# Optimization experiments

Hardware: AMD Instinct MI355X
Metric: run time of the kernel (lower is better)

The kernel has to match this reference:

```python
import jax, jax.numpy as jnp
import numpy as np

B, N, C, H = 2, 1024, 1024, 16
HD = C // H
SCALE = HD ** -0.5
TEMPERATURE = 0.8
TOP_K = 64
TOP_P = 0.9
NKAT_STRENGTH = 0.5
NKAT_DECAY = 0.95
LAYER_IDX = 2
NEG = jnp.float32(-1e9)  # stand-in for -inf; exp underflows to 0 after max-subtract


def setup_inputs() -> dict:
    key = jax.random.key(0)
    k0, k1, k2, k3 = jax.random.split(key, 4)
    x = jax.random.normal(k0, (B, N, C), dtype=jnp.float32)
    w_qkv = jax.random.normal(k1, (C, 3 * C), dtype=jnp.float32) * 0.02
    w_out = jax.random.normal(k2, (C, C), dtype=jnp.float32) * 0.02
    b_out = jnp.zeros((C,), dtype=jnp.float32)
    nkat_alpha = jnp.float32(0.1)
    nkat_beta = jnp.float32(0.05)
    return {"x": x, "w_qkv": w_qkv, "w_out": w_out, "b_out": b_out,
            "nkat_alpha": nkat_alpha, "nkat_beta": nkat_beta}


def _nkat_attention(x, w_qkv, w_out, b_out, nkat_alpha, nkat_beta):
    # qkv projection and head split
    qkv = (x @ w_qkv).reshape(B, N, 3, H, HD)
    q = jnp.transpose(qkv[:, :, 0], (0, 2, 1, 3))  # (B,H,N,HD)
    k = jnp.transpose(qkv[:, :, 1], (0, 2, 1, 3))
    v = jnp.transpose(qkv[:, :, 2], (0, 2, 1, 3))

    # scores + (zero) pos_bias + temperature scaling
    scores = jnp.einsum('bhqd,bhkd->bhqk', q, k) * SCALE
    scores = scores / max(TEMPERATURE, 1e-8)

    # top-k filtering: keep only the TOP_K largest scores per query
    kth = jax.lax.top_k(scores, TOP_K)[0][..., -1:]  # (B,H,N,1)
    scores = jnp.where(scores >= kth, scores, NEG)

    # nucleus (top-p) filtering: keep minimal prefix of sorted probs with
    # exclusive cumulative mass <= TOP_P (first element always kept)
    sorted_desc = -jnp.sort(-scores, axis=-1)
    probs = jax.nn.softmax(sorted_desc, axis=-1)
    cum = jnp.cumsum(probs, axis=-1)
    keep = (cum - probs) <= TOP_P  # exclusive cumsum <= p
    thr = jnp.min(jnp.where(keep, sorted_desc, jnp.inf), axis=-1, keepdims=True)
    scores = jnp.where(scores >= thr, scores, NEG)

    attn = jax.nn.softmax(scores, axis=-1)  # dropout p=0 -> identity (eval)

    # NKAT enhancement: per-token semantic modulation from x statistics
    layer_coeff = NKAT_STRENGTH * NKAT_DECAY ** LAYER_IDX
    token_mean = jnp.mean(x, axis=-1, keepdims=True)              # (B,N,1)
    token_var = jnp.mean((x - token_mean) ** 2, axis=-1, keepdims=True)
    theta = nkat_alpha * jnp.tanh(token_mean) + nkat_beta * jax.nn.sigmoid(token_var)
    attn = attn * (1.0 + layer_coeff * theta[:, None])            # (B,1,N,1) broadcast

    out = jnp.einsum('bhqk,bhkd->bhqd', attn, v)  # (B,H,N,HD)
    out = jnp.transpose(out, (0, 2, 1, 3)).reshape(B, N, C)
    return out @ w_out + b_out


def reference(x, w_qkv, w_out, b_out, nkat_alpha, nkat_beta):
    return _nkat_attention(x, w_qkv, w_out, b_out, nkat_alpha, nkat_beta)
```

## Files before the change

### kernel.cpp

```cpp
#include <hip/hip_runtime.h>

#define B_ 2
#define N_ 1024
#define C_ 1024
#define H_ 16
#define HD_ 64
#define KPAD 36
#define KPADL 40

typedef short short8 __attribute__((ext_vector_type(8)));
typedef float f32x4 __attribute__((ext_vector_type(4)));

union U16 {
  uint4 q;
  unsigned u[4];
  short8 s;
};

__device__ __forceinline__ float wsumf(float x) {
#pragma unroll
  for (int off = 32; off; off >>= 1) x += __shfl_xor(x, off, 64);
  return x;
}
__device__ __forceinline__ unsigned orderu(float f) {
  unsigned b = __float_as_uint(f);
  return (b & 0x80000000u) ? ~b : (b | 0x80000000u);
}
__device__ __forceinline__ float iorderu(unsigned x) {
  unsigned b = (x & 0x80000000u) ? (x & 0x7FFFFFFFu) : ~x;
  return __uint_as_float(b);
}

__device__ __forceinline__ unsigned splitf2(float f) {
  unsigned u = __float_as_uint(f);
  unsigned t = (u + 0x7fffu + ((u >> 16) & 1u)) & 0xffff0000u;
  float r = f - __uint_as_float(t);
  unsigned v = __float_as_uint(r);
  unsigned tv = v + 0x7fffu + ((v >> 16) & 1u);
  return (t >> 16) | (tv & 0xffff0000u);
}
__device__ __forceinline__ void splitf3(float f, unsigned& hm,
                                        unsigned short& lo) {
  unsigned u = __float_as_uint(f);
  unsigned t = (u + 0x7fffu + ((u >> 16) & 1u)) & 0xffff0000u;
  float r1 = f - __uint_as_float(t);
  unsigned v = __float_as_uint(r1);
  unsigned tv = (v + 0x7fffu + ((v >> 16) & 1u)) & 0xffff0000u;
  float r2 = r1 - __uint_as_float(tv);
  unsigned w = __float_as_uint(r2);
  unsigned tw = w + 0x7fffu + ((w >> 16) & 1u);
  hm = (t >> 16) | tv;
  lo = (unsigned short)(tw >> 16);
}

__device__ __forceinline__ void unpack_hm(const unsigned* p, short8& h,
                                          short8& l) {
  const uint4 X = *(const uint4*)p;
  const uint4 Y = *(const uint4*)(p + 4);
  U16 Hh, Ll;
  Hh.u[0] = (X.x & 0xffffu) | (X.y << 16);
  Hh.u[1] = (X.z & 0xffffu) | (X.w << 16);
  Hh.u[2] = (Y.x & 0xffffu) | (Y.y << 16);
  Hh.u[3] = (Y.z & 0xffffu) | (Y.w << 16);
  Ll.u[0] = (X.x >> 16) | (X.y & 0xffff0000u);
  Ll.u[1] = (X.z >> 16) | (X.w & 0xffff0000u);
  Ll.u[2] = (Y.x >> 16) | (Y.y & 0xffff0000u);
  Ll.u[3] = (Y.z >> 16) | (Y.w & 0xffff0000u);
  h = Hh.s;
  l = Ll.s;
}

__global__ __launch_bounds__(64) void factor_kernel(
    const float* __restrict__ x, const float* __restrict__ alpha_p,
    const float* __restrict__ beta_p, float* __restrict__ fac) {
  const int row = blockIdx.x;
  const int lane = threadIdx.x;
  const float4* xr = (const float4*)(x + (size_t)row * C_);
  float s = 0.f, ss = 0.f;
#pragma unroll
  for (int j = 0; j < 4; ++j) {
    float4 v = xr[lane + 64 * j];
    s += v.x + v.y + v.z + v.w;
    ss += v.x * v.x + v.y * v.y + v.z * v.z + v.w * v.w;
  }
  s = wsumf(s);
  ss = wsumf(ss);
  const float mean = s * (1.f / 1024.f);
  const float var = ss * (1.f / 1024.f) - mean * mean;
  const float theta =
      alpha_p[0] * tanhf(mean) + beta_p[0] * (1.f / (1.f + __expf(-var)));
  if (lane == 0) fac[row] = 1.f + 0.45125f * theta;
}

__device__ __forceinline__ void mfma_core6(
    const float* __restrict__ A, const float* __restrict__ Bm, int lda,
    int ldb, int m0, int n0, unsigned* a_hm, unsigned* b_hm,
    unsigned short* a_lo, unsigned short* b_lo, f32x4 acc[4][4]) {
  const int tid = threadIdx.x;
  const int lane = tid & 63;
  const int wm = ((tid >> 7) & 1) * 64;
  const int wn = ((tid >> 6) & 1) * 64;
  const int a_k4 = (tid & 7) * 4, a_m = tid >> 3;
  const int b_n4 = (tid & 31) * 4, b_k = (tid >> 5) * 4;
  const int fr = lane & 15, fk = (lane >> 4) * 8;

  float4 aR[4], bR[4];
#pragma unroll
  for (int j = 0; j < 4; ++j)
    aR[j] = *(const float4*)(A + (size_t)(m0 + a_m + 32 * j) * lda + a_k4);
#pragma unroll
  for (int i = 0; i < 4; ++i)
    bR[i] = *(const float4*)(Bm + (size_t)(b_k + i) * ldb + n0 + b_n4);

  for (int kt = 0; kt < 32; ++kt) {
    __syncthreads();
#pragma unroll
    for (int j = 0; j < 4; ++j) {
      uint4 w;
      ushort4 l;
      splitf3(aR[j].x, w.x, l.x);
      splitf3(aR[j].y, w.y, l.y);
      splitf3(aR[j].z, w.z, l.z);
      splitf3(aR[j].w, w.w, l.w);
      *(uint4*)(a_hm + (a_m + 32 * j) * KPAD + a_k4) = w;
      *(ushort4*)(a_lo + (a_m + 32 * j) * KPADL + a_k4) = l;
    }
#pragma unroll
    for (int i = 0; i < 4; ++i) {
      unsigned hm;
      unsigned short lo;
      splitf3(bR[i].x, hm, lo);
      b_hm[(b_n4 + 0) * KPAD + b_k + i] = hm;
      b_lo[(b_n4 + 0) * KPADL + b_k + i] = lo;
      splitf3(bR[i].y, hm, lo);
      b_hm[(b_n4 + 1) * KPAD + b_k + i] = hm;
      b_lo[(b_n4 + 1) * KPADL + b_k + i] = lo;
      splitf3(bR[i].z, hm, lo);
      b_hm[(b_n4 + 2) * KPAD + b_k + i] = hm;
      b_lo[(b_n4 + 2) * KPADL + b_k + i] = lo;
      splitf3(bR[i].w, hm, lo);
      b_hm[(b_n4 + 3) * KPAD + b_k + i] = hm;
      b_lo[(b_n4 + 3) * KPADL + b_k + i] = lo;
    }
    __syncthreads();
    if (kt + 1 < 32) {
      const int kb = (kt + 1) * 32;
#pragma unroll
      for (int j = 0; j < 4; ++j)
        aR[j] =
            *(const float4*)(A + (size_t)(m0 + a_m + 32 * j) * lda + kb + a_k4);
#pragma unroll
      for (int i = 0; i < 4; ++i)
        bR[i] = *(const float4*)(Bm + (size_t)(kb + b_k + i) * ldb + n0 + b_n4);
    }
    short8 ah[4], am[4], al[4];
#pragma unroll
    for (int rt = 0; rt < 4; ++rt) {
      const int row = wm + rt * 16 + fr;
      unpack_hm(a_hm + row * KPAD + fk, ah[rt], am[rt]);
      U16 L;
      L.q = *(const uint4*)(a_lo + row * KPADL + fk);
      al[rt] = L.s;
    }
#pragma unroll
    for (int ct = 0; ct < 4; ++ct) {
      const int row = wn + ct * 16 + fr;
      short8 bh, bm, bl;
      unpack_hm(b_hm + row * KPAD + fk, bh, bm);
      U16 L;
      L.q = *(const uint4*)(b_lo + row * KPADL + fk);
      bl = L.s;
#pragma unroll
      for (int rt = 0; rt < 4; ++rt) {
        f32x4 c = acc[rt][ct];
        c = __builtin_amdgcn_mfma_f32_16x16x32_bf16(ah[rt], bl, c, 0, 0, 0);
        c = __builtin_amdgcn_mfma_f32_16x16x32_bf16(al[rt], bh, c, 0, 0, 0);
        c = __builtin_amdgcn_mfma_f32_16x16x32_bf16(am[rt], bm, c, 0, 0, 0);
        c = __builtin_amdgcn_mfma_f32_16x16x32_bf16(ah[rt], bm, c, 0, 0, 0);
        c = __builtin_amdgcn_mfma_f32_16x16x32_bf16(am[rt], bh, c, 0, 0, 0);
        c = __builtin_amdgcn_mfma_f32_16x16x32_bf16(ah[rt], bh, c, 0, 0, 0);
        acc[rt][ct] = c;
      }
    }
  }
}

__device__ __forceinline__ void mfma_core3(const float* __restrict__ A,
                                           const float* __restrict__ Bm,
                                           int lda, int ldb, int m0, int n0,
                                           unsigned* a_hm, unsigned* b_hm,
                                           f32x4 acc[4][4]) {
  const int tid = threadIdx.x;
  const int lane = tid & 63;
  const int wm = ((tid >> 7) & 1) * 64;
  const int wn = ((tid >> 6) & 1) * 64;
  const int a_k4 = (tid & 7) * 4, a_m = tid >> 3;
  const int b_n4 = (tid & 31) * 4, b_k = (tid >> 5) * 4;
  const int fr = lane & 15, fk = (lane >> 4) * 8;

  float4 aR[4], bR[4];
#pragma unroll
  for (int j = 0; j < 4; ++j)
    aR[j] = *(const float4*)(A + (size_t)(m0 + a_m + 32 * j) * lda + a_k4);
#pragma unroll
  for (int i = 0; i < 4; ++i)
    bR[i] = *(const float4*)(Bm + (size_t)(b_k + i) * ldb + n0 + b_n4);

  for (int kt = 0; kt < 32; ++kt) {
    __syncthreads();
#pragma unroll
    for (int j = 0; j < 4; ++j) {
      uint4 w;
      w.x = splitf2(aR[j].x);
      w.y = splitf2(aR[j].y);
      w.z = splitf2(aR[j].z);
      w.w = splitf2(aR[j].w);
      *(uint4*)(a_hm + (a_m + 32 * j) * KPAD + a_k4) = w;
    }
#pragma unroll
    for (int i = 0; i < 4; ++i) {
      unsigned* bp = b_hm + b_k + i;
      bp[(b_n4 + 0) * KPAD] = splitf2(bR[i].x);
      bp[(b_n4 + 1) * KPAD] = splitf2(bR[i].y);
      bp[(b_n4 + 2) * KPAD] = splitf2(bR[i].z);
      bp[(b_n4 + 3) * KPAD] = splitf2(bR[i].w);
    }
    __syncthreads();
    if (kt + 1 < 32) {
      const int kb = (kt + 1) * 32;
#pragma unroll
      for (int j = 0; j < 4; ++j)
        aR[j] =
            *(const float4*)(A + (size_t)(m0 + a_m + 32 * j) * lda + kb + a_k4);
#pragma unroll
      for (int i = 0; i < 4; ++i)
        bR[i] = *(const float4*)(Bm + (size_t)(kb + b_k + i) * ldb + n0 + b_n4);
    }
    short8 ah[4], al[4];
#pragma unroll
    for (int rt = 0; rt < 4; ++rt)
      unpack_hm(a_hm + (wm + rt * 16 + fr) * KPAD + fk, ah[rt], al[rt]);
#pragma unroll
    for (int ct = 0; ct < 4; ++ct) {
      short8 bh, bl;
      unpack_hm(b_hm + (wn + ct * 16 + fr) * KPAD + fk, bh, bl);
#pragma unroll
      for (int rt = 0; rt < 4; ++rt) {
        f32x4 c = acc[rt][ct];
        c = __builtin_amdgcn_mfma_f32_16x16x32_bf16(ah[rt], bl, c, 0, 0, 0);
        c = __builtin_amdgcn_mfma_f32_16x16x32_bf16(al[rt], bh, c, 0, 0, 0);
        c = __builtin_amdgcn_mfma_f32_16x16x32_bf16(ah[rt], bh, c, 0, 0, 0);
        acc[rt][ct] = c;
      }
    }
  }
}

__global__ __launch_bounds__(256) void gemm_qk_kernel(
    const float* __restrict__ x, const float* __restrict__ w,
    float* __restrict__ q, float* __restrict__ ktb) {
  __shared__ unsigned a_hm[128 * KPAD];
  __shared__ unsigned b_hm[128 * KPAD];
  __shared__ unsigned short a_lo[128 * KPADL];
  __shared__ unsigned short b_lo[128 * KPADL];
  f32x4 acc[4][4];
#pragma unroll
  for (int i = 0; i < 4; ++i)
#pragma unroll
    for (int j = 0; j < 4; ++j) acc[i][j] = (f32x4){0.f, 0.f, 0.f, 0.f};
  const int m0 = blockIdx.y * 128, n0 = blockIdx.x * 128;
  mfma_core6(x, w, C_, 3 * C_, m0, n0, a_hm, b_hm, a_lo, b_lo, acc);

  const int lane = threadIdx.x & 63;
  const int wm = ((threadIdx.x >> 7) & 1) * 64;
  const int wn = ((threadIdx.x >> 6) & 1) * 64;
  const int rbase = (lane >> 4) * 4, cc = lane & 15;
#pragma unroll
  for (int rt = 0; rt < 4; ++rt) {
    const int m = m0 + wm + rt * 16 + rbase;
    const int bb = m >> 10, nn = m & 1023;
#pragma unroll
    for (int ct = 0; ct < 4; ++ct) {
      const int j = n0 + wn + ct * 16 + cc;
      const int sel = j >> 10, hh = (j >> 6) & 15, d0 = j & 63;
      const f32x4 c = acc[rt][ct];
      if (sel == 1) {
        *(float4*)(ktb + (((size_t)(bb * 16 + hh) * HD_ + d0) << 10) + nn) =
            make_float4(c[0], c[1], c[2], c[3]);
      } else {
        float* dst = q + (((size_t)(bb * 16 + hh) << 10) + nn) * HD_ + d0;
        dst[0] = c[0];
        dst[HD_] = c[1];
        dst[2 * HD_] = c[2];
        dst[3 * HD_] = c[3];
      }
    }
  }
}

__global__ __launch_bounds__(256) void gemm_v_kernel(
    const float* __restrict__ x, const float* __restrict__ w,
    float* __restrict__ v) {
  __shared__ unsigned a_hm[128 * KPAD];
  __shared__ unsigned b_hm[128 * KPAD];
  f32x4 acc[4][4];
#pragma unroll
  for (int i = 0; i < 4; ++i)
#pragma unroll
    for (int j = 0; j < 4; ++j) acc[i][j] = (f32x4){0.f, 0.f, 0.f, 0.f};
  const int m0 = blockIdx.y * 128, n0 = 2048 + blockIdx.x * 128;
  mfma_core3(x, w, C_, 3 * C_, m0, n0, a_hm, b_hm, acc);

  const int lane = threadIdx.x & 63;
  const int wm = ((threadIdx.x >> 7) & 1) * 64;
  const int wn = ((threadIdx.x >> 6) & 1) * 64;
  const int rbase = (lane >> 4) * 4, cc = lane & 15;
#pragma unroll
  for (int rt = 0; rt < 4; ++rt) {
    const int m = m0 + wm + rt * 16 + rbase;
    const int bb = m >> 10, nn = m & 1023;
#pragma unroll
    for (int ct = 0; ct < 4; ++ct) {
      const int jv = (n0 - 2048) + wn + ct * 16 + cc;
      const int hh = (jv >> 6) & 15, d0 = jv & 63;
      const f32x4 c = acc[rt][ct];
      float* dst = v + (((size_t)(bb * 16 + hh) << 10) + nn) * HD_ + d0;
      dst[0] = c[0];
      dst[HD_] = c[1];
      dst[2 * HD_] = c[2];
      dst[3 * HD_] = c[3];
    }
  }
}

__global__ __launch_bounds__(256) void gemm_out_kernel(
    const float* __restrict__ a, const float* __restrict__ w,
    const float* __restrict__ bias, float* __restrict__ out) {
  __shared__ unsigned a_hm[128 * KPAD];
  __shared__ unsigned b_hm[128 * KPAD];
  f32x4 acc[4][4];
#pragma unroll
  for (int i = 0; i < 4; ++i)
#pragma unroll
    for (int j = 0; j < 4; ++j) acc[i][j] = (f32x4){0.f, 0.f, 0.f, 0.f};
  const int m0 = blockIdx.y * 128, n0 = blockIdx.x * 128;
  mfma_core3(a, w, C_, C_, m0, n0, a_hm, b_hm, acc);

  const int lane = threadIdx.x & 63;
  const int wm = ((threadIdx.x >> 7) & 1) * 64;
  const int wn = ((threadIdx.x >> 6) & 1) * 64;
  const int rbase = (lane >> 4) * 4, cc = lane & 15;
#pragma unroll
  for (int rt = 0; rt < 4; ++rt) {
    const int m = m0 + wm + rt * 16 + rbase;
#pragma unroll
    for (int ct = 0; ct < 4; ++ct) {
      const int j = n0 + wn + ct * 16 + cc;
      const float bj = bias[j];
      const f32x4 c = acc[rt][ct];
      float* dst = out + (size_t)m * C_ + j;
      dst[0] = c[0] + bj;
      dst[C_] = c[1] + bj;
      dst[2 * C_] = c[2] + bj;
      dst[3 * C_] = c[3] + bj;
    }
  }
}

__global__ __launch_bounds__(256) void attn_kernel(
    const float* __restrict__ qw, const float* __restrict__ kt,
    const float* __restrict__ vw, const float* __restrict__ fac,
    float* __restrict__ ao) {
  const int lane = threadIdx.x & 63;
  const int wid = threadIdx.x >> 6;
  const int qblk = blockIdx.x * 16;
  const int bh = qblk >> 10;
  const int b = bh >> 4, h = bh & 15;
  const int q0 = (qblk & (N_ - 1)) + wid * 4;

  __shared__ __align__(16) float q_ldsT[4][HD_][4];
  __shared__ unsigned su[4][64];
  __shared__ float sv[4][64];
  __shared__ int ck[4][64];
  __shared__ float cv[4][64];

  {
    const int qq = lane >> 4, dp = (lane & 15) << 2;
    const float4 v =
        *(const float4*)(qw + ((size_t)bh * N_ + q0 + qq) * HD_ + dp);
    q_ldsT[wid][dp + 0][qq] = v.x;
    q_ldsT[wid][dp + 1][qq] = v.y;
    q_ldsT[wid][dp + 2][qq] = v.z;
    q_ldsT[wid][dp + 3][qq] = v.w;
  }

  const float* ktb = kt + ((size_t)bh * HD_ * N_);
  const unsigned long long ltmask = (1ull << lane) - 1ull;
  unsigned u[4][16];

  for (int pass = 0; pass < 4; ++pass) {
    float acc[4][4];
#pragma unroll
    for (int a = 0; a < 4; ++a)
#pragma unroll
      for (int c = 0; c < 4; ++c) acc[a][c] = 0.f;
    const float* kp = ktb + (pass << 8) + (lane << 2);
#pragma unroll 4
    for (int d = 0; d < HD_; ++d) {
      const float4 kv = *(const float4*)(kp + (size_t)d * N_);
      const float4 qv = *(const float4*)(&q_ldsT[wid][d][0]);
      acc[0][0] = fmaf(kv.x, qv.x, acc[0][0]);
      acc[0][1] = fmaf(kv.x, qv.y, acc[0][1]);
      acc[0][2] = fmaf(kv.x, qv.z, acc[0][2]);
      acc[0][3] = fmaf(kv.x, qv.w, acc[0][3]);
      acc[1][0] = fmaf(kv.y, qv.x, acc[1][0]);
      acc[1][1] = fmaf(kv.y, qv.y, acc[1][1]);
      acc[1][2] = fmaf(kv.y, qv.z, acc[1][2]);
      acc[1][3] = fmaf(kv.y, qv.w, acc[1][3]);
      acc[2][0] = fmaf(kv.z, qv.x, acc[2][0]);
      acc[2][1] = fmaf(kv.z, qv.y, acc[2][1]);
      acc[2][2] = fmaf(kv.z, qv.z, acc[2][2]);
      acc[2][3] = fmaf(kv.z, qv.w, acc[2][3]);
      acc[3][0] = fmaf(kv.w, qv.x, acc[3][0]);
      acc[3][1] = fmaf(kv.w, qv.y, acc[3][1]);
      acc[3][2] = fmaf(kv.w, qv.z, acc[3][2]);
      acc[3][3] = fmaf(kv.w, qv.w, acc[3][3]);
    }
#pragma unroll
    for (int jl = 0; jl < 4; ++jl)
#pragma unroll
      for (int q = 0; q < 4; ++q)
        u[q][(pass << 2) + jl] = orderu((acc[jl][q] * 0.125f) / 0.8f);
  }

  unsigned mu[4], l0[4];
#pragma unroll
  for (int q = 0; q < 4; ++q) {
    unsigned mq = u[q][0];
#pragma unroll
    for (int j = 1; j < 16; ++j) mq = max(mq, u[q][j]);
    mu[q] = mq;
    l0[q] = mq;
  }
#pragma unroll
  for (int off = 32; off; off >>= 1) {
#pragma unroll
    for (int q = 0; q < 4; ++q) {
      mu[q] = max(mu[q], (unsigned)__shfl_xor((int)mu[q], off, 64));
      l0[q] = min(l0[q], (unsigned)__shfl_xor((int)l0[q], off, 64));
    }
  }

  unsigned lo[4], hi[4];
#pragma unroll
  for (int q = 0; q < 4; ++q) {
    lo[q] = l0[q];
    hi[q] = mu[q];
  }
  while ((lo[0] < hi[0]) | (lo[1] < hi[1]) | (lo[2] < hi[2]) |
         (lo[3] < hi[3])) {
#pragma unroll
    for (int q = 0; q < 4; ++q) {
      if (lo[q] < hi[q]) {
        const unsigned mid = lo[q] + ((hi[q] - lo[q]) >> 1) + 1u;
        int c = 0;
#pragma unroll
        for (int j = 0; j < 16; ++j)
          c += (int)__popcll(__ballot(u[q][j] >= mid));
        if (c >= 64) lo[q] = mid;
        else hi[q] = mid - 1u;
      }
    }
  }

  const float* vb = vw + ((size_t)bh << 16);
#pragma unroll
  for (int qq = 0; qq < 4; ++qq) {
    const unsigned kthu = lo[qq];
    const float m = iorderu(mu[qq]);

    float e[16];
    float zl = 0.f;
#pragma unroll
    for (int j = 0; j < 16; ++j) {
      const float ej = (u[qq][j] >= kthu) ? __expf(iorderu(u[qq][j]) - m) : 0.f;
      e[j] = ej;
      zl += ej;
    }
    const float Z = wsumf(zl);
    const float limit = 0.9f * Z;

    int base = 0;
#pragma unroll
    for (int j = 0; j < 16; ++j) {
      const bool f = (u[qq][j] >= kthu);
      const unsigned long long mb = __ballot(f);
      if (f) {
        const int pos = base + (int)__popcll(mb & ltmask);
        if (pos < 64) {
          su[wid][pos] = u[qq][j];
          sv[wid][pos] = e[j];
        }
      }
      base += (int)__popcll(mb);
    }

    unsigned sk = ~su[wid][lane];
    float se = sv[wid][lane];
#pragma unroll
    for (int k = 2; k <= 64; k <<= 1) {
#pragma unroll
      for (int j = k >> 1; j; j >>= 1) {
        const unsigned pk = (unsigned)__shfl_xor((int)sk, j, 64);
        const float pe = __shfl_xor(se, j, 64);
        const bool takeMin = (((lane & j) == 0) == ((lane & k) == 0));
        const bool sw = takeMin ? (pk < sk) : (pk > sk);
        if (sw) {
          sk = pk;
          se = pe;
        }
      }
    }

    float pre = se;
#pragma unroll
    for (int off = 1; off <= 32; off <<= 1) {
      const float t = __shfl_up(pre, off, 64);
      if (lane >= off) pre += t;
    }
    const float excl = pre - se;
    const bool keep = (excl <= limit);
    const unsigned long long km = __ballot(keep);
    const int L = 63 - __builtin_clzll(km);
    const unsigned thr = ~(unsigned)__shfl((int)sk, L, 64);

    float z2l = 0.f;
#pragma unroll
    for (int j = 0; j < 16; ++j) z2l += (u[qq][j] >= thr) ? e[j] : 0.f;
    const float Z2 = wsumf(z2l);
    const float wsc = fac[(b << 10) + q0 + qq] / Z2;

    int M = 0;
#pragma unroll
    for (int j = 0; j < 16; ++j) {
      const bool f = (u[qq][j] >= thr);
      const unsigned long long mb = __ballot(f);
      if (f) {
        const int pos = M + (int)__popcll(mb & ltmask);
        if (pos < 64) {
          ck[wid][pos] = ((j >> 2) << 8) + (lane << 2) + (j & 3);
          cv[wid][pos] = e[j] * wsc;
        }
      }
      M += (int)__popcll(mb);
    }
    if (M > 64) M = 64;

    float a0 = 0.f, a1 = 0.f, a2 = 0.f, a3 = 0.f;
    int i = 0;
    for (; i + 4 <= M; i += 4) {
      const int k0 = ck[wid][i], k1 = ck[wid][i + 1];
      const int k2 = ck[wid][i + 2], k3 = ck[wid][i + 3];
      const float c0 = cv[wid][i], c1 = cv[wid][i + 1];
      const float c2 = cv[wid][i + 2], c3 = cv[wid][i + 3];
      a0 = fmaf(c0, vb[((size_t)k0 << 6) + lane], a0);
      a1 = fmaf(c1, vb[((size_t)k1 << 6) + lane], a1);
      a2 = fmaf(c2, vb[((size_t)k2 << 6) + lane], a2);
      a3 = fmaf(c3, vb[((size_t)k3 << 6) + lane], a3);
    }
    for (; i < M; ++i)
      a0 = fmaf(cv[wid][i], vb[((size_t)ck[wid][i] << 6) + lane], a0);
    const float o = (a0 + a1) + (a2 + a3);

    ao[(((size_t)b << 10) + q0 + qq) * C_ + (h << 6) + lane] = o;
  }
}

extern "C" void kernel_launch(void* const* d_in, const int* in_sizes, int n_in,
                              void* d_out, int out_size, void* d_ws,
                              size_t ws_size, hipStream_t stream) {
  const float* x = (const float*)d_in[0];
  const float* wqkv = (const float*)d_in[1];
  const float* wout = (const float*)d_in[2];
  const float* bout = (const float*)d_in[3];
  const float* alpha = (const float*)d_in[4];
  const float* beta = (const float*)d_in[5];
  float* out = (float*)d_out;

  float* ws = (float*)d_ws;
  const size_t SZ = (size_t)B_ * H_ * N_ * HD_;
  float* qw = ws;
  float* kt = ws + SZ;
  float* vw = ws + 2 * SZ;
  float* ao = ws + 3 * SZ;
  float* fc = ws + 4 * SZ;

  factor_kernel<<<B_ * N_, 64, 0, stream>>>(x, alpha, beta, fc);
  gemm_qk_kernel<<<dim3(16, 16), 256, 0, stream>>>(x, wqkv, qw, kt);
  gemm_v_kernel<<<dim3(8, 16), 256, 0, stream>>>(x, wqkv, vw);
  attn_kernel<<<(B_ * H_ * N_) / 16, 256, 0, stream>>>(qw, kt, vw, fc, ao);
  gemm_out_kernel<<<dim3(8, 16), 256, 0, stream>>>(ao, wout, bout, out);
}
```

Baseline: 447.3 us.

## Pre-split fp32 operands into bf16 planes before the GEMMs

Adds separate kernels that split x and the transposed weights into high/mid/low bf16 planes once, so the GEMM main loops only copy ready-made bf16 tiles into shared memory instead of splitting and scattering fp32 values per tile. The attention kernel now writes its output directly as two bf16 planes for the output projection. This removes repeated split arithmetic and the strided shared-memory transpose stores from the GEMM inner loops. The cost is extra kernel launches and extra global traffic to write and reread the split planes, plus a larger workspace layout with buffers reused through aliasing.

```diff
diff --git a/kernel.cpp b/kernel.cpp
--- a/kernel.cpp
+++ b/kernel.cpp
@@ -5,17 +5,11 @@
 #define C_ 1024
 #define H_ 16
 #define HD_ 64
-#define KPAD 36
-#define KPADL 40
+#define PK 40
 
 typedef short short8 __attribute__((ext_vector_type(8)));
 typedef float f32x4 __attribute__((ext_vector_type(4)));
-
-union U16 {
-  uint4 q;
-  unsigned u[4];
-  short8 s;
-};
+typedef unsigned short ushort_t;
 
 __device__ __forceinline__ float wsumf(float x) {
 #pragma unroll
@@ -39,8 +33,7 @@
   unsigned tv = v + 0x7fffu + ((v >> 16) & 1u);
   return (t >> 16) | (tv & 0xffff0000u);
 }
-__device__ __forceinline__ void splitf3(float f, unsigned& hm,
-                                        unsigned short& lo) {
+__device__ __forceinline__ void splitf3(float f, unsigned& hm, ushort_t& lo) {
   unsigned u = __float_as_uint(f);
   unsigned t = (u + 0x7fffu + ((u >> 16) & 1u)) & 0xffff0000u;
   float r1 = f - __uint_as_float(t);
@@ -50,24 +43,7 @@
   unsigned w = __float_as_uint(r2);
   unsigned tw = w + 0x7fffu + ((w >> 16) & 1u);
   hm = (t >> 16) | tv;
-  lo = (unsigned short)(tw >> 16);
-}
-
-__device__ __forceinline__ void unpack_hm(const unsigned* p, short8& h,
-                                          short8& l) {
-  const uint4 X = *(const uint4*)p;
-  const uint4 Y = *(const uint4*)(p + 4);
-  U16 Hh, Ll;
-  Hh.u[0] = (X.x & 0xffffu) | (X.y << 16);
-  Hh.u[1] = (X.z & 0xffffu) | (X.w << 16);
-  Hh.u[2] = (Y.x & 0xffffu) | (Y.y << 16);
-  Hh.u[3] = (Y.z & 0xffffu) | (Y.w << 16);
-  Ll.u[0] = (X.x >> 16) | (X.y & 0xffff0000u);
-  Ll.u[1] = (X.z >> 16) | (X.w & 0xffff0000u);
-  Ll.u[2] = (Y.x >> 16) | (Y.y & 0xffff0000u);
-  Ll.u[3] = (Y.z >> 16) | (Y.w & 0xffff0000u);
-  h = Hh.s;
-  l = Ll.s;
+  lo = (ushort_t)(tw >> 16);
 }
 
 __global__ __launch_bounds__(64) void factor_kernel(
@@ -92,203 +68,173 @@
   if (lane == 0) fac[row] = 1.f + 0.45125f * theta;
 }
 
-__device__ __forceinline__ void mfma_core6(
-    const float* __restrict__ A, const float* __restrict__ Bm, int lda,
-    int ldb, int m0, int n0, unsigned* a_hm, unsigned* b_hm,
-    unsigned short* a_lo, unsigned short* b_lo, f32x4 acc[4][4]) {
+__global__ __launch_bounds__(256) void split_x_kernel(
+    const float* __restrict__ x, ushort_t* __restrict__ xh,
+    ushort_t* __restrict__ xm, ushort_t* __restrict__ xl) {
+  const int i = (blockIdx.x * 256 + threadIdx.x) * 4;
+  const float4 v = *(const float4*)(x + i);
+  unsigned hm0, hm1, hm2, hm3;
+  ushort_t l0, l1, l2, l3;
+  splitf3(v.x, hm0, l0);
+  splitf3(v.y, hm1, l1);
+  splitf3(v.z, hm2, l2);
+  splitf3(v.w, hm3, l3);
+  *(ushort4*)(xh + i) =
+      make_ushort4(hm0 & 0xffffu, hm1 & 0xffffu, hm2 & 0xffffu, hm3 & 0xffffu);
+  *(ushort4*)(xm + i) =
+      make_ushort4(hm0 >> 16, hm1 >> 16, hm2 >> 16, hm3 >> 16);
+  *(ushort4*)(xl + i) = make_ushort4(l0, l1, l2, l3);
+}
+
+__global__ __launch_bounds__(256) void split_wT_kernel(
+    const float* __restrict__ src, int ldsrc, ushort_t* __restrict__ th,
+    ushort_t* __restrict__ tm, ushort_t* __restrict__ tl) {
+  __shared__ float tile[64][65];
+  const int t = threadIdx.x;
+  const int k0 = blockIdx.y * 64, j0 = blockIdx.x * 64;
+  const int rr = t >> 4, cc4 = (t & 15) * 4;
+#pragma unroll
+  for (int p = 0; p < 4; ++p) {
+    const float4 v =
+        *(const float4*)(src + (size_t)(k0 + rr + 16 * p) * ldsrc + j0 + cc4);
+    tile[rr + 16 * p][cc4 + 0] = v.x;
+    tile[rr + 16 * p][cc4 + 1] = v.y;
+    tile[rr + 16 * p][cc4 + 2] = v.z;
+    tile[rr + 16 * p][cc4 + 3] = v.w;
+  }
+  __syncthreads();
+  const int j = t >> 2, kc = (t & 3) * 16;
+#pragma unroll
+  for (int half = 0; half < 2; ++half) {
+    unsigned hw[4], mw[4], lw[4];
+#pragma unroll
+    for (int e = 0; e < 4; ++e) {
+      unsigned hmA, hmB;
+      ushort_t loA, loB;
+      splitf3(tile[kc + half * 8 + 2 * e][j], hmA, loA);
+      splitf3(tile[kc + half * 8 + 2 * e + 1][j], hmB, loB);
+      hw[e] = (hmA & 0xffffu) | ((hmB & 0xffffu) << 16);
+      mw[e] = (hmA >> 16) | (hmB & 0xffff0000u);
+      lw[e] = (unsigned)loA | ((unsigned)loB << 16);
+    }
+    const size_t o = (size_t)(j0 + j) * 1024 + k0 + kc + half * 8;
+    *(uint4*)(th + o) = make_uint4(hw[0], hw[1], hw[2], hw[3]);
+    *(uint4*)(tm + o) = make_uint4(mw[0], mw[1], mw[2], mw[3]);
+    *(uint4*)(tl + o) = make_uint4(lw[0], lw[1], lw[2], lw[3]);
+  }
+}
+
+__global__ __launch_bounds__(256) void gemm_qk_kernel(
+    const ushort_t* __restrict__ xh, const ushort_t* __restrict__ xm,
+    const ushort_t* __restrict__ xl, const ushort_t* __restrict__ wh,
+    const ushort_t* __restrict__ wm, const ushort_t* __restrict__ wl,
+    float* __restrict__ q, float* __restrict__ ktb) {
+  __shared__ ushort_t Ah[128 * PK], Am[128 * PK], Al[128 * PK];
+  __shared__ ushort_t Bh[128 * PK], Bm2[128 * PK], Bl[128 * PK];
+  f32x4 acc[4][4];
+#pragma unroll
+  for (int i = 0; i < 4; ++i)
+#pragma unroll
+    for (int j = 0; j < 4; ++j) acc[i][j] = (f32x4){0.f, 0.f, 0.f, 0.f};
   const int tid = threadIdx.x;
   const int lane = tid & 63;
-  const int wm = ((tid >> 7) & 1) * 64;
-  const int wn = ((tid >> 6) & 1) * 64;
-  const int a_k4 = (tid & 7) * 4, a_m = tid >> 3;
-  const int b_n4 = (tid & 31) * 4, b_k = (tid >> 5) * 4;
+  const int m0 = blockIdx.y * 128, n0 = blockIdx.x * 128;
+  const int wro = ((tid >> 7) & 1) * 64;
+  const int wco = ((tid >> 6) & 1) * 64;
+  const int srow = tid >> 1, soff = (tid & 1) * 16;
   const int fr = lane & 15, fk = (lane >> 4) * 8;
-
-  float4 aR[4], bR[4];
-#pragma unroll
-  for (int j = 0; j < 4; ++j)
-    aR[j] = *(const float4*)(A + (size_t)(m0 + a_m + 32 * j) * lda + a_k4);
-#pragma unroll
-  for (int i = 0; i < 4; ++i)
-    bR[i] = *(const float4*)(Bm + (size_t)(b_k + i) * ldb + n0 + b_n4);
-
+  const size_t ga = (size_t)(m0 + srow) * 1024 + soff;
+  const size_t gb = (size_t)(n0 + srow) * 1024 + soff;
+
+  uint4 aR[3][2], bR[3][2];
+  aR[0][0] = *(const uint4*)(xh + ga);
+  aR[0][1] = *(const uint4*)(xh + ga + 8);
+  aR[1][0] = *(const uint4*)(xm + ga);
+  aR[1][1] = *(const uint4*)(xm + ga + 8);
+  aR[2][0] = *(const uint4*)(xl + ga);
+  aR[2][1] = *(const uint4*)(xl + ga + 8);
+  bR[0][0] = *(const uint4*)(wh + gb);
+  bR[0][1] = *(const uint4*)(wh + gb + 8);
+  bR[1][0] = *(const uint4*)(wm + gb);
+  bR[1][1] = *(const uint4*)(wm + gb + 8);
+  bR[2][0] = *(const uint4*)(wl + gb);
+  bR[2][1] = *(const uint4*)(wl + gb + 8);
+
+  const int lbase = srow * PK + soff;
   for (int kt = 0; kt < 32; ++kt) {
     __syncthreads();
-#pragma unroll
-    for (int j = 0; j < 4; ++j) {
-      uint4 w;
-      ushort4 l;
-      splitf3(aR[j].x, w.x, l.x);
-      splitf3(aR[j].y, w.y, l.y);
-      splitf3(aR[j].z, w.z, l.z);
-      splitf3(aR[j].w, w.w, l.w);
-      *(uint4*)(a_hm + (a_m + 32 * j) * KPAD + a_k4) = w;
-      *(ushort4*)(a_lo + (a_m + 32 * j) * KPADL + a_k4) = l;
-    }
-#pragma unroll
-    for (int i = 0; i < 4; ++i) {
-      unsigned hm;
-      unsigned short lo;
-      splitf3(bR[i].x, hm, lo);
-      b_hm[(b_n4 + 0) * KPAD + b_k + i] = hm;
-      b_lo[(b_n4 + 0) * KPADL + b_k + i] = lo;
-      splitf3(bR[i].y, hm, lo);
-      b_hm[(b_n4 + 1) * KPAD + b_k + i] = hm;
-      b_lo[(b_n4 + 1) * KPADL + b_k + i] = lo;
-      splitf3(bR[i].z, hm, lo);
-      b_hm[(b_n4 + 2) * KPAD + b_k + i] = hm;
-      b_lo[(b_n4 + 2) * KPADL + b_k + i] = lo;
-      splitf3(bR[i].w, hm, lo);
-      b_hm[(b_n4 + 3) * KPAD + b_k + i] = hm;
-      b_lo[(b_n4 + 3) * KPADL + b_k + i] = lo;
-    }
+    *(uint4*)&Ah[lbase] = aR[0][0];
+    *(uint4*)&Ah[lbase + 8] = aR[0][1];
+    *(uint4*)&Am[lbase] = aR[1][0];
+    *(uint4*)&Am[lbase + 8] = aR[1][1];
+    *(uint4*)&Al[lbase] = aR[2][0];
+    *(uint4*)&Al[lbase + 8] = aR[2][1];
+    *(uint4*)&Bh[lbase] = bR[0][0];
+    *(uint4*)&Bh[lbase + 8] = bR[0][1];
+    *(uint4*)&Bm2[lbase] = bR[1][0];
+    *(uint4*)&Bm2[lbase + 8] = bR[1][1];
+    *(uint4*)&Bl[lbase] = bR[2][0];
+    *(uint4*)&Bl[lbase + 8] = bR[2][1];
     __syncthreads();
     if (kt + 1 < 32) {
-      const int kb = (kt + 1) * 32;
-#pragma unroll
-      for (int j = 0; j < 4; ++j)
-        aR[j] =
-            *(const float4*)(A + (size_t)(m0 + a_m + 32 * j) * lda + kb + a_k4);
-#pragma unroll
-      for (int i = 0; i < 4; ++i)
-        bR[i] = *(const float4*)(Bm + (size_t)(kb + b_k + i) * ldb + n0 + b_n4);
-    }
-    short8 ah[4], am[4], al[4];
+      const size_t oa = ga + (size_t)(kt + 1) * 32;
+      const size_t ob = gb + (size_t)(kt + 1) * 32;
+      aR[0][0] = *(const uint4*)(xh + oa);
+      aR[0][1] = *(const uint4*)(xh + oa + 8);
+      aR[1][0] = *(const uint4*)(xm + oa);
+      aR[1][1] = *(const uint4*)(xm + oa + 8);
+      aR[2][0] = *(const uint4*)(xl + oa);
+      aR[2][1] = *(const uint4*)(xl + oa + 8);
+      bR[0][0] = *(const uint4*)(wh + ob);
+      bR[0][1] = *(const uint4*)(wh + ob + 8);
+      bR[1][0] = *(const uint4*)(wm + ob);
+      bR[1][1] = *(const uint4*)(wm + ob + 8);
+      bR[2][0] = *(const uint4*)(wl + ob);
+      bR[2][1] = *(const uint4*)(wl + ob + 8);
+    }
+    short8 fah[4], fam[4], fal[4];
 #pragma unroll
     for (int rt = 0; rt < 4; ++rt) {
-      const int row = wm + rt * 16 + fr;
-      unpack_hm(a_hm + row * KPAD + fk, ah[rt], am[rt]);
-      U16 L;
-      L.q = *(const uint4*)(a_lo + row * KPADL + fk);
-      al[rt] = L.s;
+      const int ba = (wro + rt * 16 + fr) * PK + fk;
+      fah[rt] = *(const short8*)&Ah[ba];
+      fam[rt] = *(const short8*)&Am[ba];
+      fal[rt] = *(const short8*)&Al[ba];
     }
 #pragma unroll
     for (int ct = 0; ct < 4; ++ct) {
-      const int row = wn + ct * 16 + fr;
-      short8 bh, bm, bl;
-      unpack_hm(b_hm + row * KPAD + fk, bh, bm);
-      U16 L;
-      L.q = *(const uint4*)(b_lo + row * KPADL + fk);
-      bl = L.s;
+      const int bb = (wco + ct * 16 + fr) * PK + fk;
+      const short8 fbh = *(const short8*)&Bh[bb];
+      const short8 fbm = *(const short8*)&Bm2[bb];
+      const short8 fbl = *(const short8*)&Bl[bb];
 #pragma unroll
       for (int rt = 0; rt < 4; ++rt) {
         f32x4 c = acc[rt][ct];
-        c = __builtin_amdgcn_mfma_f32_16x16x32_bf16(ah[rt], bl, c, 0, 0, 0);
-        c = __builtin_amdgcn_mfma_f32_16x16x32_bf16(al[rt], bh, c, 0, 0, 0);
-        c = __builtin_amdgcn_mfma_f32_16x16x32_bf16(am[rt], bm, c, 0, 0, 0);
-        c = __builtin_amdgcn_mfma_f32_16x16x32_bf16(ah[rt], bm, c, 0, 0, 0);
-        c = __builtin_amdgcn_mfma_f32_16x16x32_bf16(am[rt], bh, c, 0, 0, 0);
-        c = __builtin_amdgcn_mfma_f32_16x16x32_bf16(ah[rt], bh, c, 0, 0, 0);
+        c = __builtin_amdgcn_mfma_f32_16x16x32_bf16(fah[rt], fbl, c, 0, 0, 0);
+        c = __builtin_amdgcn_mfma_f32_16x16x32_bf16(fal[rt], fbh, c, 0, 0, 0);
+        c = __builtin_amdgcn_mfma_f32_16x16x32_bf16(fam[rt], fbm, c, 0, 0, 0);
+        c = __builtin_amdgcn_mfma_f32_16x16x32_bf16(fah[rt], fbm, c, 0, 0, 0);
+        c = __builtin_amdgcn_mfma_f32_16x16x32_bf16(fam[rt], fbh, c, 0, 0, 0);
+        c = __builtin_amdgcn_mfma_f32_16x16x32_bf16(fah[rt], fbh, c, 0, 0, 0);
         acc[rt][ct] = c;
       }
     }
   }
-}
-
-__device__ __forceinline__ void mfma_core3(const float* __restrict__ A,
-                                           const float* __restrict__ Bm,
-                                           int lda, int ldb, int m0, int n0,
-                                           unsigned* a_hm, unsigned* b_hm,
-                                           f32x4 acc[4][4]) {
-  const int tid = threadIdx.x;
-  const int lane = tid & 63;
-  const int wm = ((tid >> 7) & 1) * 64;
-  const int wn = ((tid >> 6) & 1) * 64;
-  const int a_k4 = (tid & 7) * 4, a_m = tid >> 3;
-  const int b_n4 = (tid & 31) * 4, b_k = (tid >> 5) * 4;
-  const int fr = lane & 15, fk = (lane >> 4) * 8;
-
-  float4 aR[4], bR[4];
-#pragma unroll
-  for (int j = 0; j < 4; ++j)
-    aR[j] = *(const float4*)(A + (size_t)(m0 + a_m + 32 * j) * lda + a_k4);
-#pragma unroll
-  for (int i = 0; i < 4; ++i)
-    bR[i] = *(const float4*)(Bm + (size_t)(b_k + i) * ldb + n0 + b_n4);
-
-  for (int kt = 0; kt < 32; ++kt) {
-    __syncthreads();
-#pragma unroll
-    for (int j = 0; j < 4; ++j) {
-      uint4 w;
-      w.x = splitf2(aR[j].x);
-      w.y = splitf2(aR[j].y);
-      w.z = splitf2(aR[j].z);
-      w.w = splitf2(aR[j].w);
-      *(uint4*)(a_hm + (a_m + 32 * j) * KPAD + a_k4) = w;
-    }
-#pragma unroll
-    for (int i = 0; i < 4; ++i) {
-      unsigned* bp = b_hm + b_k + i;
-      bp[(b_n4 + 0) * KPAD] = splitf2(bR[i].x);
-      bp[(b_n4 + 1) * KPAD] = splitf2(bR[i].y);
-      bp[(b_n4 + 2) * KPAD] = splitf2(bR[i].z);
-      bp[(b_n4 + 3) * KPAD] = splitf2(bR[i].w);
-    }
-    __syncthreads();
-    if (kt + 1 < 32) {
-      const int kb = (kt + 1) * 32;
-#pragma unroll
-      for (int j = 0; j < 4; ++j)
-        aR[j] =
-            *(const float4*)(A + (size_t)(m0 + a_m + 32 * j) * lda + kb + a_k4);
-#pragma unroll
-      for (int i = 0; i < 4; ++i)
-        bR[i] = *(const float4*)(Bm + (size_t)(kb + b_k + i) * ldb + n0 + b_n4);
-    }
-    short8 ah[4], al[4];
-#pragma unroll
-    for (int rt = 0; rt < 4; ++rt)
-      unpack_hm(a_hm + (wm + rt * 16 + fr) * KPAD + fk, ah[rt], al[rt]);
+
+  const int rbase = (lane >> 4) * 4, cc = lane & 15;
+#pragma unroll
+  for (int rt = 0; rt < 4; ++rt) {
+    const int m = m0 + wro + rt * 16 + rbase;
+    const int bb2 = m >> 10, nn = m & 1023;
 #pragma unroll
     for (int ct = 0; ct < 4; ++ct) {
-      short8 bh, bl;
-      unpack_hm(b_hm + (wn + ct * 16 + fr) * KPAD + fk, bh, bl);
-#pragma unroll
-      for (int rt = 0; rt < 4; ++rt) {
-        f32x4 c = acc[rt][ct];
-        c = __builtin_amdgcn_mfma_f32_16x16x32_bf16(ah[rt], bl, c, 0, 0, 0);
-        c = __builtin_amdgcn_mfma_f32_16x16x32_bf16(al[rt], bh, c, 0, 0, 0);
-        c = __builtin_amdgcn_mfma_f32_16x16x32_bf16(ah[rt], bh, c, 0, 0, 0);
-        acc[rt][ct] = c;
-      }
-    }
-  }
-}
-
-__global__ __launch_bounds__(256) void gemm_qk_kernel(
-    const float* __restrict__ x, const float* __restrict__ w,
-    float* __restrict__ q, float* __restrict__ ktb) {
-  __shared__ unsigned a_hm[128 * KPAD];
-  __shared__ unsigned b_hm[128 * KPAD];
-  __shared__ unsigned short a_lo[128 * KPADL];
-  __shared__ unsigned short b_lo[128 * KPADL];
-  f32x4 acc[4][4];
-#pragma unroll
-  for (int i = 0; i < 4; ++i)
-#pragma unroll
-    for (int j = 0; j < 4; ++j) acc[i][j] = (f32x4){0.f, 0.f, 0.f, 0.f};
-  const int m0 = blockIdx.y * 128, n0 = blockIdx.x * 128;
-  mfma_core6(x, w, C_, 3 * C_, m0, n0, a_hm, b_hm, a_lo, b_lo, acc);
-
-  const int lane = threadIdx.x & 63;
-  const int wm = ((threadIdx.x >> 7) & 1) * 64;
-  const int wn = ((threadIdx.x >> 6) & 1) * 64;
-  const int rbase = (lane >> 4) * 4, cc = lane & 15;
-#pragma unroll
-  for (int rt = 0; rt < 4; ++rt) {
-    const int m = m0 + wm + rt * 16 + rbase;
-    const int bb = m >> 10, nn = m & 1023;
-#pragma unroll
-    for (int ct = 0; ct < 4; ++ct) {
-      const int j = n0 + wn + ct * 16 + cc;
+      const int j = n0 + wco + ct * 16 + cc;
       const int sel = j >> 10, hh = (j >> 6) & 15, d0 = j & 63;
       const f32x4 c = acc[rt][ct];
       if (sel == 1) {
-        *(float4*)(ktb + (((size_t)(bb * 16 + hh) * HD_ + d0) << 10) + nn) =
+        *(float4*)(ktb + (((size_t)(bb2 * 16 + hh) * HD_ + d0) << 10) + nn) =
             make_float4(c[0], c[1], c[2], c[3]);
       } else {
-        float* dst = q + (((size_t)(bb * 16 + hh) << 10) + nn) * HD_ + d0;
+        float* dst = q + (((size_t)(bb2 * 16 + hh) << 10) + nn) * HD_ + d0;
         dst[0] = c[0];
         dst[HD_] = c[1];
         dst[2 * HD_] = c[2];
@@ -298,30 +244,103 @@
   }
 }
 
+__device__ __forceinline__ void mfma_core3p(
+    const ushort_t* __restrict__ Ahp, const ushort_t* __restrict__ Amp,
+    const ushort_t* __restrict__ Bhp, const ushort_t* __restrict__ Bmp,
+    int m0, int n0, ushort_t* Ah, ushort_t* Am, ushort_t* Bh, ushort_t* Bm2,
+    f32x4 acc[4][4]) {
+  const int tid = threadIdx.x;
+  const int lane = tid & 63;
+  const int wro = ((tid >> 7) & 1) * 64;
+  const int wco = ((tid >> 6) & 1) * 64;
+  const int srow = tid >> 1, soff = (tid & 1) * 16;
+  const int fr = lane & 15, fk = (lane >> 4) * 8;
+  const size_t ga = (size_t)(m0 + srow) * 1024 + soff;
+  const size_t gb = (size_t)(n0 + srow) * 1024 + soff;
+
+  uint4 aR[2][2], bR[2][2];
+  aR[0][0] = *(const uint4*)(Ahp + ga);
+  aR[0][1] = *(const uint4*)(Ahp + ga + 8);
+  aR[1][0] = *(const uint4*)(Amp + ga);
+  aR[1][1] = *(const uint4*)(Amp + ga + 8);
+  bR[0][0] = *(const uint4*)(Bhp + gb);
+  bR[0][1] = *(const uint4*)(Bhp + gb + 8);
+  bR[1][0] = *(const uint4*)(Bmp + gb);
+  bR[1][1] = *(const uint4*)(Bmp + gb + 8);
+
+  const int lbase = srow * PK + soff;
+  for (int kt = 0; kt < 32; ++kt) {
+    __syncthreads();
+    *(uint4*)&Ah[lbase] = aR[0][0];
+    *(uint4*)&Ah[lbase + 8] = aR[0][1];
+    *(uint4*)&Am[lbase] = aR[1][0];
+    *(uint4*)&Am[lbase + 8] = aR[1][1];
+    *(uint4*)&Bh[lbase] = bR[0][0];
+    *(uint4*)&Bh[lbase + 8] = bR[0][1];
+    *(uint4*)&Bm2[lbase] = bR[1][0];
+    *(uint4*)&Bm2[lbase + 8] = bR[1][1];
+    __syncthreads();
+    if (kt + 1 < 32) {
+      const size_t oa = ga + (size_t)(kt + 1) * 32;
+      const size_t ob = gb + (size_t)(kt + 1) * 32;
+      aR[0][0] = *(const uint4*)(Ahp + oa);
+      aR[0][1] = *(const uint4*)(Ahp + oa + 8);
+      aR[1][0] = *(const uint4*)(Amp + oa);
+      aR[1][1] = *(const uint4*)(Amp + oa + 8);
+      bR[0][0] = *(const uint4*)(Bhp + ob);
+      bR[0][1] = *(const uint4*)(Bhp + ob + 8);
+      bR[1][0] = *(const uint4*)(Bmp + ob);
+      bR[1][1] = *(const uint4*)(Bmp + ob + 8);
+    }
+    short8 fah[4], fam[4];
+#pragma unroll
+    for (int rt = 0; rt < 4; ++rt) {
+      const int ba = (wro + rt * 16 + fr) * PK + fk;
+      fah[rt] = *(const short8*)&Ah[ba];
+      fam[rt] = *(const short8*)&Am[ba];
+    }
+#pragma unroll
+    for (int ct = 0; ct < 4; ++ct) {
+      const int bb = (wco + ct * 16 + fr) * PK + fk;
+      const short8 fbh = *(const short8*)&Bh[bb];
+      const short8 fbm = *(const short8*)&Bm2[bb];
+#pragma unroll
+      for (int rt = 0; rt < 4; ++rt) {
+        f32x4 c = acc[rt][ct];
+        c = __builtin_amdgcn_mfma_f32_16x16x32_bf16(fah[rt], fbm, c, 0, 0, 0);
+        c = __builtin_amdgcn_mfma_f32_16x16x32_bf16(fam[rt], fbh, c, 0, 0, 0);
+        c = __builtin_amdgcn_mfma_f32_16x16x32_bf16(fah[rt], fbh, c, 0, 0, 0);
+        acc[rt][ct] = c;
+      }
+    }
+  }
+}
+
 __global__ __launch_bounds__(256) void gemm_v_kernel(
-    const float* __restrict__ x, const float* __restrict__ w,
+    const ushort_t* __restrict__ xh, const ushort_t* __restrict__ xm,
+    const ushort_t* __restrict__ wh, const ushort_t* __restrict__ wm,
     float* __restrict__ v) {
-  __shared__ unsigned a_hm[128 * KPAD];
-  __shared__ unsigned b_hm[128 * KPAD];
+  __shared__ ushort_t Ah[128 * PK], Am[128 * PK];
+  __shared__ ushort_t Bh[128 * PK], Bm2[128 * PK];
   f32x4 acc[4][4];
 #pragma unroll
   for (int i = 0; i < 4; ++i)
 #pragma unroll
     for (int j = 0; j < 4; ++j) acc[i][j] = (f32x4){0.f, 0.f, 0.f, 0.f};
   const int m0 = blockIdx.y * 128, n0 = 2048 + blockIdx.x * 128;
-  mfma_core3(x, w, C_, 3 * C_, m0, n0, a_hm, b_hm, acc);
+  mfma_core3p(xh, xm, wh, wm, m0, n0, Ah, Am, Bh, Bm2, acc);
 
   const int lane = threadIdx.x & 63;
-  const int wm = ((threadIdx.x >> 7) & 1) * 64;
-  const int wn = ((threadIdx.x >> 6) & 1) * 64;
+  const int wro = ((threadIdx.x >> 7) & 1) * 64;
+  const int wco = ((threadIdx.x >> 6) & 1) * 64;
   const int rbase = (lane >> 4) * 4, cc = lane & 15;
 #pragma unroll
   for (int rt = 0; rt < 4; ++rt) {
-    const int m = m0 + wm + rt * 16 + rbase;
+    const int m = m0 + wro + rt * 16 + rbase;
     const int bb = m >> 10, nn = m & 1023;
 #pragma unroll
     for (int ct = 0; ct < 4; ++ct) {
-      const int jv = (n0 - 2048) + wn + ct * 16 + cc;
+      const int jv = (n0 - 2048) + wco + ct * 16 + cc;
       const int hh = (jv >> 6) & 15, d0 = jv & 63;
       const f32x4 c = acc[rt][ct];
       float* dst = v + (((size_t)(bb * 16 + hh) << 10) + nn) * HD_ + d0;
@@ -334,28 +353,29 @@
 }
 
 __global__ __launch_bounds__(256) void gemm_out_kernel(
-    const float* __restrict__ a, const float* __restrict__ w,
+    const ushort_t* __restrict__ aoh, const ushort_t* __restrict__ aom,
+    const ushort_t* __restrict__ wh, const ushort_t* __restrict__ wm,
     const float* __restrict__ bias, float* __restrict__ out) {
-  __shared__ unsigned a_hm[128 * KPAD];
-  __shared__ unsigned b_hm[128 * KPAD];
+  __shared__ ushort_t Ah[128 * PK], Am[128 * PK];
+  __shared__ ushort_t Bh[128 * PK], Bm2[128 * PK];
   f32x4 acc[4][4];
 #pragma unroll
   for (int i = 0; i < 4; ++i)
 #pragma unroll
     for (int j = 0; j < 4; ++j) acc[i][j] = (f32x4){0.f, 0.f, 0.f, 0.f};
   const int m0 = blockIdx.y * 128, n0 = blockIdx.x * 128;
-  mfma_core3(a, w, C_, C_, m0, n0, a_hm, b_hm, acc);
+  mfma_core3p(aoh, aom, wh, wm, m0, n0, Ah, Am, Bh, Bm2, acc);
 
   const int lane = threadIdx.x & 63;
-  const int wm = ((threadIdx.x >> 7) & 1) * 64;
-  const int wn = ((threadIdx.x >> 6) & 1) * 64;
+  const int wro = ((threadIdx.x >> 7) & 1) * 64;
+  const int wco = ((threadIdx.x >> 6) & 1) * 64;
   const int rbase = (lane >> 4) * 4, cc = lane & 15;
 #pragma unroll
   for (int rt = 0; rt < 4; ++rt) {
-    const int m = m0 + wm + rt * 16 + rbase;
+    const int m = m0 + wro + rt * 16 + rbase;
 #pragma unroll
     for (int ct = 0; ct < 4; ++ct) {
-      const int j = n0 + wn + ct * 16 + cc;
+      const int j = n0 + wco + ct * 16 + cc;
       const float bj = bias[j];
       const f32x4 c = acc[rt][ct];
       float* dst = out + (size_t)m * C_ + j;
@@ -370,7 +390,7 @@
 __global__ __launch_bounds__(256) void attn_kernel(
     const float* __restrict__ qw, const float* __restrict__ kt,
     const float* __restrict__ vw, const float* __restrict__ fac,
-    float* __restrict__ ao) {
+    ushort_t* __restrict__ aoh, ushort_t* __restrict__ aom) {
   const int lane = threadIdx.x & 63;
   const int wid = threadIdx.x >> 6;
   const int qblk = blockIdx.x * 16;
@@ -572,7 +592,10 @@
       a0 = fmaf(cv[wid][i], vb[((size_t)ck[wid][i] << 6) + lane], a0);
     const float o = (a0 + a1) + (a2 + a3);
 
-    ao[(((size_t)b << 10) + q0 + qq) * C_ + (h << 6) + lane] = o;
+    const unsigned pk2 = splitf2(o);
+    const size_t idx = (((size_t)b << 10) + q0 + qq) * C_ + (h << 6) + lane;
+    aoh[idx] = (ushort_t)(pk2 & 0xffffu);
+    aom[idx] = (ushort_t)(pk2 >> 16);
   }
 }
 
@@ -588,16 +611,33 @@
   float* out = (float*)d_out;
 
   float* ws = (float*)d_ws;
-  const size_t SZ = (size_t)B_ * H_ * N_ * HD_;
+  const size_t M1 = 1u << 20;
   float* qw = ws;
-  float* kt = ws + SZ;
-  float* vw = ws + 2 * SZ;
-  float* ao = ws + 3 * SZ;
-  float* fc = ws + 4 * SZ;
-
+  float* kt = ws + 2 * M1;
+  float* vw = ws + 4 * M1;
+  float* fc = ws + 6 * M1;
+  ushort_t* xh = (ushort_t*)(ws + 6 * M1 + 4096);
+  ushort_t* xm = (ushort_t*)(ws + 7 * M1 + 4096);
+  ushort_t* xl = (ushort_t*)(ws + 8 * M1 + 4096);
+  ushort_t* wqh = (ushort_t*)(ws + 9 * M1 + 4096);
+  ushort_t* wqm = (ushort_t*)(ws + 10 * M1 + 4096 + M1 / 2);
+  ushort_t* wql = (ushort_t*)(ws + 12 * M1 + 4096);
+  ushort_t* woh = wql;
+  ushort_t* wom = wql + M1;
+  ushort_t* wol = wql + 2 * M1;
+  ushort_t* aoh = xh;
+  ushort_t* aom = xm;
+
+  split_x_kernel<<<2048, 256, 0, stream>>>(x, xh, xm, xl);
+  split_wT_kernel<<<dim3(48, 16), 256, 0, stream>>>(wqkv, 3 * C_, wqh, wqm,
+                                                    wql);
   factor_kernel<<<B_ * N_, 64, 0, stream>>>(x, alpha, beta, fc);
-  gemm_qk_kernel<<<dim3(16, 16), 256, 0, stream>>>(x, wqkv, qw, kt);
-  gemm_v_kernel<<<dim3(8, 16), 256, 0, stream>>>(x, wqkv, vw);
-  attn_kernel<<<(B_ * H_ * N_) / 16, 256, 0, stream>>>(qw, kt, vw, fc, ao);
-  gemm_out_kernel<<<dim3(8, 16), 256, 0, stream>>>(ao, wout, bout, out);
-}
+  gemm_qk_kernel<<<dim3(16, 16), 256, 0, stream>>>(xh, xm, xl, wqh, wqm, wql,
+                                                   qw, kt);
+  gemm_v_kernel<<<dim3(8, 16), 256, 0, stream>>>(xh, xm, wqh, wqm, vw);
+  split_wT_kernel<<<dim3(16, 16), 256, 0, stream>>>(wout, C_, woh, wom, wol);
+  attn_kernel<<<(B_ * H_ * N_) / 16, 256, 0, stream>>>(qw, kt, vw, fc, aoh,
+                                                       aom);
+  gemm_out_kernel<<<dim3(8, 16), 256, 0, stream>>>(aoh, aom, woh, wom, bout,
+                                                   out);
+}
```

After: 577.1 us. +29.0%, slower.
